# Kernel optimization log

Hardware: AMD Instinct MI355X
Metric: run time of the kernel (lower is better)

The kernel has to match this reference:

```python
import jax, jax.numpy as jnp
import numpy as np

N_PER_GRAPH = 468
B = 32
N = B * N_PER_GRAPH            # 14976 nodes
E = 89600                      # synthetic Delaunay-like directed edges
IN_DIM, HID, OUT, HEADS = 2, 256, 512, 4
NEG_SLOPE = 0.2
EPS = 1e-16


def setup_inputs() -> dict:
    key = jax.random.key(0)
    ks = jax.random.split(key, 12)
    x = jax.random.uniform(ks[0], (N, IN_DIM), dtype=jnp.float32)
    edge_index = jax.random.randint(ks[1], (2, E), 0, N, dtype=jnp.int64)
    batch = jnp.repeat(jnp.arange(B, dtype=jnp.int64), N_PER_GRAPH)
    s1 = 1.0 / np.sqrt(IN_DIM)
    s2 = 1.0 / np.sqrt(HID)
    sg = 1.0 / np.sqrt(OUT)
    return {
        "x": x,
        "edge_index": edge_index,
        "batch": batch,
        # GATConv 1: in_dim -> hidden, heads=4, concat=False
        "W1": jax.random.normal(ks[2], (IN_DIM, HEADS * HID), jnp.float32) * s1,
        "a1_src": jax.random.normal(ks[3], (HEADS, HID), jnp.float32) * s2,
        "a1_dst": jax.random.normal(ks[4], (HEADS, HID), jnp.float32) * s2,
        "b1": jnp.zeros((HID,), jnp.float32),
        # GATConv 2: hidden -> out, heads=4, concat=False
        "W2": jax.random.normal(ks[5], (HID, HEADS * OUT), jnp.float32) * s2,
        "a2_src": jax.random.normal(ks[6], (HEADS, OUT), jnp.float32) * sg,
        "a2_dst": jax.random.normal(ks[7], (HEADS, OUT), jnp.float32) * sg,
        "b2": jnp.zeros((OUT,), jnp.float32),
        # GlobalAttention gate_nn: Linear(out_dim, 1)
        "Wg": jax.random.normal(ks[8], (OUT, 1), jnp.float32) * sg,
        "bg": jnp.zeros((1,), jnp.float32),
    }


def _gat_layer(x, src, dst, W, a_src, a_dst, b, heads, out_ch):
    n = x.shape[0]
    xh = (x @ W).reshape(n, heads, out_ch)            # [N,H,C]
    alpha_s = jnp.einsum("nhc,hc->nh", xh, a_src)     # [N,H]
    alpha_d = jnp.einsum("nhc,hc->nh", xh, a_dst)
    e = alpha_s[src] + alpha_d[dst]                   # [E,H]
    e = jnp.where(e > 0, e, NEG_SLOPE * e)            # leaky_relu(0.2)
    # segment softmax over incoming edges of each destination node
    m = jax.ops.segment_max(e, dst, num_segments=n)
    ex = jnp.exp(e - m[dst])
    denom = jax.ops.segment_sum(ex, dst, num_segments=n)
    alpha = ex / (denom[dst] + EPS)                   # [E,H]
    msg = xh[src] * alpha[:, :, None]                 # [E,H,C]
    out = jax.ops.segment_sum(msg, dst, num_segments=n)  # [N,H,C]
    return out.mean(axis=1) + b                       # concat=False -> head mean


def reference(x, edge_index, batch, W1, a1_src, a1_dst, b1,
              W2, a2_src, a2_dst, b2, Wg, bg):
    n = x.shape[0]
    # PyG GATConv default add_self_loops=True (both layers use the same graph)
    loops = jnp.arange(n, dtype=edge_index.dtype)
    src = jnp.concatenate([edge_index[0], loops])
    dst = jnp.concatenate([edge_index[1], loops])

    h = _gat_layer(x, src, dst, W1, a1_src, a1_dst, b1, HEADS, HID)
    h = jax.nn.relu(h)
    h = _gat_layer(h, src, dst, W2, a2_src, a2_dst, b2, HEADS, OUT)
    h = jax.nn.relu(h)

    # GlobalAttention pooling: gate = Linear(out,1), softmax per graph, weighted sum
    gate = h @ Wg + bg                                # [N,1]
    gm = jax.ops.segment_max(gate, batch, num_segments=B)
    ge = jnp.exp(gate - gm[batch])
    gs = jax.ops.segment_sum(ge, batch, num_segments=B)
    attn = ge / (gs[batch] + EPS)                     # [N,1]
    pooled = jax.ops.segment_sum(attn * h, batch, num_segments=B)  # [B,512]
    return pooled.reshape(-1, 1, OUT)                 # [B,1,512]
```

## Files before the change

### kernel.cpp

```cpp
#include <hip/hip_runtime.h>
#include <hip/hip_bf16.h>
#include <math.h>

#define HEADS 4
#define C1 256
#define C2 512
#define NEG 0.2f
#define EPSF 1e-16f
#define DCAP 64

using bf16x8 = __attribute__((ext_vector_type(8))) short;
using f32x4  = __attribute__((ext_vector_type(4))) float;

__device__ __forceinline__ float lrelu(float e) { return e > 0.f ? e : NEG * e; }

__device__ __forceinline__ unsigned short f2bf(float v) {
    __hip_bfloat16 b = __float2bfloat16(v);
    return *reinterpret_cast<unsigned short*>(&b);
}
__device__ __forceinline__ float bf2f(unsigned short u) {
    __hip_bfloat16 b = *reinterpret_cast<__hip_bfloat16*>(&u);
    return __bfloat162float(b);
}


__global__ __launch_bounds__(256) void k1_prep(
    const float* __restrict__ x, const float* __restrict__ W1,
    const float* __restrict__ a1s, const float* __restrict__ a1d,
    const float* __restrict__ W2, const float* __restrict__ a2s, const float* __restrict__ a2d,
    const int* __restrict__ ei, int E, int N,
    float* __restrict__ as1, float* __restrict__ ad1,
    float* __restrict__ w2a,
    unsigned short* __restrict__ W2t_hi, unsigned short* __restrict__ W2t_lo,
    int* __restrict__ deg, int* __restrict__ bucket)
{
    int b = blockIdx.x, tid = threadIdx.x;
    int wv = tid >> 6, lane = tid & 63;
    if (b < 59) {
        __shared__ float s_w1a[16];
#pragma unroll
        for (int q = 0; q < 4; q++) {
            int o = wv * 4 + q, sd = o >> 3, idx = o & 7, h = idx >> 1, d = idx & 1;
            const float* av = sd ? a1d : a1s;
            float p = 0.f;
            for (int c = lane; c < 256; c += 64) p += W1[d * 1024 + h * 256 + c] * av[h * 256 + c];
#pragma unroll
            for (int m = 32; m >= 1; m >>= 1) p += __shfl_xor(p, m, 64);
            if (lane == 0) s_w1a[o] = p;
        }
        __syncthreads();
        int n = b * 256 + tid;
        if (n < N) {
            float x0 = x[2 * n], x1 = x[2 * n + 1];
            float4 av, dv;
            float* ap = &av.x; float* dp = &dv.x;
#pragma unroll
            for (int h = 0; h < 4; h++) {
                ap[h] = x0 * s_w1a[h * 2] + x1 * s_w1a[h * 2 + 1];
                dp[h] = x0 * s_w1a[8 + h * 2] + x1 * s_w1a[8 + h * 2 + 1];
            }
            *reinterpret_cast<float4*>(&as1[n * 4]) = av;
            *reinterpret_cast<float4*>(&ad1[n * 4]) = dv;
        }
    } else if (b < 67) {
        int bb = b - 59, sd = bb >> 2, h = bb & 3;
        const float* av = sd ? a2d : a2s;
        float gv[8];
#pragma unroll
        for (int q = 0; q < 8; q++) gv[q] = av[h * 512 + lane * 8 + q];
        for (int k = wv; k < 256; k += 4) {
            const float4 w0 = *reinterpret_cast<const float4*>(&W2[(size_t)k * 2048 + h * 512 + lane * 8]);
            const float4 w1 = *reinterpret_cast<const float4*>(&W2[(size_t)k * 2048 + h * 512 + lane * 8 + 4]);
            float p = w0.x*gv[0] + w0.y*gv[1] + w0.z*gv[2] + w0.w*gv[3]
                    + w1.x*gv[4] + w1.y*gv[5] + w1.z*gv[6] + w1.w*gv[7];
#pragma unroll
            for (int m = 32; m >= 1; m >>= 1) p += __shfl_xor(p, m, 64);
            if (lane == 0) w2a[sd * 1024 + h * 256 + k] = p;
        }
    } else if (b < 195) {
        __shared__ float T[64][65];
        int lin = b - 67;
        int kk0 = (lin & 15) * 64, n0 = (lin >> 4) * 64;
        int h = kk0 >> 8, k0 = kk0 & 255;
#pragma unroll
        for (int rr = 0; rr < 16; rr++) {
            int ki = rr * 4 + (tid >> 6), ni = tid & 63;
            T[ki][ni] = W2[(size_t)(k0 + ki) * 2048 + h * 512 + n0 + ni];
        }
        __syncthreads();
#pragma unroll
        for (int rr = 0; rr < 16; rr++) {
            int ni = rr * 4 + (tid >> 6), ki = tid & 63;
            float v = T[ki][ni];
            unsigned short hi = f2bf(v);
            unsigned short lo = f2bf(v - bf2f(hi));
            int rowp = n0 + ni, kg = kk0 + ki;
            int kt = kg >> 5, cb = rowp >> 4;
            int ll = (rowp & 15) | (((kg >> 3) & 3) << 4);
            size_t o = ((size_t)(kt * 32 + cb) * 64 + ll) * 8 + (kg & 7);
            W2t_hi[o] = hi; W2t_lo[o] = lo;
        }
    } else {
        int i = (b - 195) * 256 + tid;
        if (i < E) {
            int s = ei[i], d = ei[E + i];
            int slot = atomicAdd(&deg[d], 1);
            if (slot < DCAP) bucket[d * DCAP + slot] = s;
        }
    }
}

__global__ __launch_bounds__(256) void k4_agg1_h1(
    const float* __restrict__ x, const float* __restrict__ as1, const float* __restrict__ ad1,
    const int* __restrict__ deg, const int* __restrict__ bucket,
    const float* __restrict__ W1, const float* __restrict__ b1, const float* __restrict__ w2a,
    float* __restrict__ h1, float* __restrict__ as2, float* __restrict__ ad2)
{
    int wv = threadIdx.x >> 6, lane = threadIdx.x & 63;
    int n = blockIdx.x * 4 + wv;
    const float4 sa4 = *reinterpret_cast<const float4*>(&as1[n * 4]);
    const float4 da4 = *reinterpret_cast<const float4*>(&ad1[n * 4]);
    const float sa[4] = {sa4.x, sa4.y, sa4.z, sa4.w};
    const float da[4] = {da4.x, da4.y, da4.z, da4.w};
    float acc[8] = {0,0,0,0,0,0,0,0};
    float den[4] = {0,0,0,0};
    int dg = min(deg[n], DCAP);
    for (int i = lane; i < dg; i += 64) {
        int s = bucket[n * DCAP + i];
        const float4 a4 = *reinterpret_cast<const float4*>(&as1[s * 4]);
        const float af[4] = {a4.x, a4.y, a4.z, a4.w};
        const float2 xv = reinterpret_cast<const float2*>(x)[s];
#pragma unroll
        for (int q = 0; q < 4; q++) {
            float w = expf(lrelu(af[q] + da[q]));
            den[q] += w;
            acc[2 * q]     = fmaf(w, xv.x, acc[2 * q]);
            acc[2 * q + 1] = fmaf(w, xv.y, acc[2 * q + 1]);
        }
    }
#pragma unroll
    for (int msk = 1; msk <= 32; msk <<= 1) {
#pragma unroll
        for (int q = 0; q < 8; q++) acc[q] += __shfl_xor(acc[q], msk, 64);
#pragma unroll
        for (int q = 0; q < 4; q++) den[q] += __shfl_xor(den[q], msk, 64);
    }
    const float2 xn = reinterpret_cast<const float2*>(x)[n];
    float xa[8];
#pragma unroll
    for (int q = 0; q < 4; q++) {
        float ws = expf(lrelu(sa[q] + da[q]));
        float dq = den[q] + ws;
        float inv = 1.f / (dq + EPSF);
        xa[2 * q]     = (acc[2 * q]     + ws * xn.x) * inv;
        xa[2 * q + 1] = (acc[2 * q + 1] + ws * xn.y) * inv;
    }
    float t[4] = {0.f, 0.f, 0.f, 0.f};
#pragma unroll
    for (int h = 0; h < 4; h++)
#pragma unroll
        for (int d = 0; d < 2; d++) {
            const float4 w4 = *reinterpret_cast<const float4*>(&W1[d * 1024 + h * 256 + lane * 4]);
            float xx = xa[h * 2 + d];
            t[0] = fmaf(xx, w4.x, t[0]);
            t[1] = fmaf(xx, w4.y, t[1]);
            t[2] = fmaf(xx, w4.z, t[2]);
            t[3] = fmaf(xx, w4.w, t[3]);
        }
    const float4 b4 = *reinterpret_cast<const float4*>(&b1[lane * 4]);
    float v[4];
    v[0] = fmaxf(fmaf(0.25f, t[0], b4.x), 0.f);
    v[1] = fmaxf(fmaf(0.25f, t[1], b4.y), 0.f);
    v[2] = fmaxf(fmaf(0.25f, t[2], b4.z), 0.f);
    v[3] = fmaxf(fmaf(0.25f, t[3], b4.w), 0.f);
    *reinterpret_cast<float4*>(&h1[(size_t)n * 256 + lane * 4]) = make_float4(v[0], v[1], v[2], v[3]);
    float p[8];
#pragma unroll
    for (int o = 0; o < 8; o++) {
        int sd = o >> 2, h = o & 3;
        const float4 w4 = *reinterpret_cast<const float4*>(&w2a[sd * 1024 + h * 256 + lane * 4]);
        p[o] = v[0] * w4.x + v[1] * w4.y + v[2] * w4.z + v[3] * w4.w;
    }
#pragma unroll
    for (int msk = 1; msk <= 32; msk <<= 1)
#pragma unroll
        for (int o = 0; o < 8; o++) p[o] += __shfl_xor(p[o], msk, 64);
    if (lane == 0) {
        *reinterpret_cast<float4*>(&as2[n * 4]) = make_float4(p[0], p[1], p[2], p[3]);
        *reinterpret_cast<float4*>(&ad2[n * 4]) = make_float4(p[4], p[5], p[6], p[7]);
    }
}

__global__ __launch_bounds__(256) void k6_agg2(
    const float* __restrict__ h1, const float* __restrict__ as2, const float* __restrict__ ad2,
    const int* __restrict__ deg, const int* __restrict__ bucket,
    unsigned short* __restrict__ hagg_hi, unsigned short* __restrict__ hagg_lo, int nrb)
{
    int wv = threadIdx.x >> 6, lane = threadIdx.x & 63;
    int n = blockIdx.x * 4 + wv;
    const float4 sa4 = *reinterpret_cast<const float4*>(&as2[n * 4]);
    const float4 da4 = *reinterpret_cast<const float4*>(&ad2[n * 4]);
    const float sa[4] = {sa4.x, sa4.y, sa4.z, sa4.w};
    const float da[4] = {da4.x, da4.y, da4.z, da4.w};
    float den[4], acc[4][4];
    const float4 hs = *reinterpret_cast<const float4*>(&h1[(size_t)n * 256 + lane * 4]);
    const float hv0[4] = {hs.x, hs.y, hs.z, hs.w};
#pragma unroll
    for (int h = 0; h < 4; h++) {
        float ws = expf(lrelu(sa[h] + da[h]));
        den[h] = ws;
#pragma unroll
        for (int q = 0; q < 4; q++) acc[h][q] = ws * hv0[q];
    }
    int dg = min(deg[n], DCAP);
    for (int i = 0; i < dg; i++) {
        int s = bucket[n * DCAP + i];
        const float4 a4 = *reinterpret_cast<const float4*>(&as2[s * 4]);
        const float af[4] = {a4.x, a4.y, a4.z, a4.w};
        const float4 hv = *reinterpret_cast<const float4*>(&h1[(size_t)s * 256 + lane * 4]);
#pragma unroll
        for (int h = 0; h < 4; h++) {
            float w = expf(lrelu(af[h] + da[h]));
            den[h] += w;
            acc[h][0] = fmaf(w, hv.x, acc[h][0]);
            acc[h][1] = fmaf(w, hv.y, acc[h][1]);
            acc[h][2] = fmaf(w, hv.z, acc[h][2]);
            acc[h][3] = fmaf(w, hv.w, acc[h][3]);
        }
    }
    int rb = n >> 4;
    int ll = (n & 15) | (((lane >> 1) & 3) << 4);
    int jj0 = (lane & 1) * 4;
#pragma unroll
    for (int h = 0; h < 4; h++) {
        float inv = 1.f / (den[h] + EPSF);
        ushort4 hi4, lo4;
        unsigned short* hp = &hi4.x; unsigned short* lp = &lo4.x;
#pragma unroll
        for (int q = 0; q < 4; q++) {
            float val = acc[h][q] * inv;
            unsigned short hi = f2bf(val);
            hp[q] = hi;
            lp[q] = f2bf(val - bf2f(hi));
        }
        int kt = h * 8 + (lane >> 3);
        size_t o = ((size_t)(kt * nrb + rb) * 64 + ll) * 8 + jj0;
        *reinterpret_cast<ushort4*>(&hagg_hi[o]) = hi4;
        *reinterpret_cast<ushort4*>(&hagg_lo[o]) = lo4;
    }
}

#define K7_PREF(S, KT) do { int _ao = aoff + (KT) * astep, _bo = boff + (KT) * 2048; \
    _Pragma("unroll") for (int i = 0; i < 4; i++) { \
        S##ah[i] = pAh[_ao + i * 64]; S##al[i] = pAl[_ao + i * 64]; \
        S##bh[i] = pBh[_bo + i * 64]; S##bl[i] = pBl[_bo + i * 64]; } } while (0)

#define K7_MFMA(S) do { _Pragma("unroll") for (int i = 0; i < 4; i++) \
    _Pragma("unroll") for (int jj = 0; jj < 4; jj++) { \
        acc[i][jj] = __builtin_amdgcn_mfma_f32_16x16x32_bf16(S##ah[i], S##bh[jj], acc[i][jj], 0, 0, 0); \
        acc[i][jj] = __builtin_amdgcn_mfma_f32_16x16x32_bf16(S##ah[i], S##bl[jj], acc[i][jj], 0, 0, 0); \
        acc[i][jj] = __builtin_amdgcn_mfma_f32_16x16x32_bf16(S##al[i], S##bh[jj], acc[i][jj], 0, 0, 0); } } while (0)

__global__ __launch_bounds__(256) void k7_gemm2(
    const unsigned short* __restrict__ Ahi, const unsigned short* __restrict__ Alo,
    const unsigned short* __restrict__ Bhi, const unsigned short* __restrict__ Blo,
    const float* __restrict__ b2, const float* __restrict__ Wg,
    float* __restrict__ h2, float* __restrict__ gate, int nrb)
{
    __shared__ float s_gate[128];
    int tid = threadIdx.x, l = tid & 63, wv = tid >> 6;
    int wr = wv >> 1, wc = wv & 1;
    int bid = blockIdx.x, rtile, ctile;
    if (bid < 448) { rtile = (bid & 7) + 8 * (bid >> 5); ctile = (bid >> 3) & 3; }
    else           { int t = bid - 448; rtile = 112 + (t >> 2); ctile = t & 3; }
    int row0 = rtile * 128, col0 = ctile * 128;
    int lm = l & 15, lg = l >> 4;
    if (tid < 128) s_gate[tid] = 0.f;

    const bf16x8* pAh = (const bf16x8*)Ahi;
    const bf16x8* pAl = (const bf16x8*)Alo;
    const bf16x8* pBh = (const bf16x8*)Bhi;
    const bf16x8* pBl = (const bf16x8*)Blo;
    int aoff = (rtile * 8 + wr * 4) * 64 + l;
    int boff = (ctile * 8 + wc * 4) * 64 + l;
    const int astep = nrb * 64;

    f32x4 acc[4][4];
#pragma unroll
    for (int i = 0; i < 4; i++)
#pragma unroll
        for (int jj = 0; jj < 4; jj++) { acc[i][jj][0]=0.f; acc[i][jj][1]=0.f; acc[i][jj][2]=0.f; acc[i][jj][3]=0.f; }

    bf16x8 pah[4], pal[4], pbh[4], pbl[4];
    bf16x8 qah[4], qal[4], qbh[4], qbl[4];
    K7_PREF(p, 0);
    for (int kt = 0; kt < 32; kt += 2) {
        K7_PREF(q, kt + 1);
        K7_MFMA(p);
        if (kt + 2 < 32) K7_PREF(p, kt + 2);
        K7_MFMA(q);
    }
    __syncthreads();

    float b2c[4], wgj[4];
#pragma unroll
    for (int jj = 0; jj < 4; jj++) {
        int col = col0 + wc * 64 + jj * 16 + lm;
        b2c[jj] = b2[col]; wgj[jj] = Wg[col];
    }
#pragma unroll
    for (int i = 0; i < 4; i++) {
#pragma unroll
        for (int r = 0; r < 4; r++) {
            int row = row0 + wr * 64 + i * 16 + lg * 4 + r;
            float g = 0.f;
#pragma unroll
            for (int jj = 0; jj < 4; jj++) {
                float v = fmaxf(fmaf(0.25f, acc[i][jj][r], b2c[jj]), 0.f);
                h2[(size_t)row * 512 + col0 + wc * 64 + jj * 16 + lm] = v;
                g = fmaf(v, wgj[jj], g);
            }
            g += __shfl_xor(g, 1, 64);
            g += __shfl_xor(g, 2, 64);
            g += __shfl_xor(g, 4, 64);
            g += __shfl_xor(g, 8, 64);
            if (lm == 0) atomicAdd(&s_gate[wr * 64 + i * 16 + lg * 4 + r], g);
        }
    }
    __syncthreads();
    if (tid < 128) atomicAdd(&gate[row0 + tid], s_gate[tid]);
}

__global__ __launch_bounds__(256) void k8_pool(
    const float* __restrict__ gate, const float* __restrict__ h2,
    float* __restrict__ out, int npg)
{
    int bq = blockIdx.x, cs = blockIdx.y, tid = threadIdx.x;
    int n0 = bq * npg;
    __shared__ float sw[512];
    __shared__ float sred[4];
    __shared__ float4 sacc[256];
    float part = 0.f;
    for (int i = tid; i < 512; i += 256) {
        float e = (i < npg) ? expf(gate[n0 + i]) : 0.f;
        sw[i] = e; part += e;
    }
#pragma unroll
    for (int m = 32; m >= 1; m >>= 1) part += __shfl_xor(part, m, 64);
    if ((tid & 63) == 0) sred[tid >> 6] = part;
    __syncthreads();
    float inv = 1.f / (sred[0] + sred[1] + sred[2] + sred[3] + EPSF);
    int slot = tid & 31, sub = tid >> 5;
    const float* base = h2 + (size_t)n0 * 512 + cs * 128 + slot * 4;
    float4 acc = make_float4(0.f, 0.f, 0.f, 0.f);
    for (int i = sub; i < npg; i += 8) {
        float w = sw[i];
        const float4 v = *reinterpret_cast<const float4*>(base + (size_t)i * 512);
        acc.x = fmaf(w, v.x, acc.x);
        acc.y = fmaf(w, v.y, acc.y);
        acc.z = fmaf(w, v.z, acc.z);
        acc.w = fmaf(w, v.w, acc.w);
    }
    sacc[tid] = acc;
    __syncthreads();
    if (sub == 0) {
        float4 t = acc;
#pragma unroll
        for (int s2 = 1; s2 < 8; s2++) {
            const float4 o = sacc[s2 * 32 + slot];
            t.x += o.x; t.y += o.y; t.z += o.z; t.w += o.w;
        }
        t.x *= inv; t.y *= inv; t.z *= inv; t.w *= inv;
        *reinterpret_cast<float4*>(&out[(size_t)bq * 512 + cs * 128 + slot * 4]) = t;
    }
}

extern "C" void kernel_launch(void* const* d_in, const int* in_sizes, int n_in,
                              void* d_out, int out_size, void* d_ws, size_t ws_size,
                              hipStream_t stream)
{
    const float* x    = (const float*)d_in[0];
    const int*   ei   = (const int*)d_in[1];
    const float* W1   = (const float*)d_in[3];
    const float* a1s  = (const float*)d_in[4];
    const float* a1d  = (const float*)d_in[5];
    const float* b1   = (const float*)d_in[6];
    const float* W2   = (const float*)d_in[7];
    const float* a2s  = (const float*)d_in[8];
    const float* a2d  = (const float*)d_in[9];
    const float* b2   = (const float*)d_in[10];
    const float* Wg   = (const float*)d_in[11];
    float* out = (float*)d_out;

    const int N = in_sizes[0] / 2;
    const int E = in_sizes[1] / 2;
    const int Bq = out_size / C2;
    const int npg = N / Bq;
    const int nrb = N >> 4;

    char* w = (char*)d_ws;
    size_t off = 0;
    auto alloc = [&](size_t bytes) { void* p = w + off; off += (bytes + 255) & ~(size_t)255; return p; };

    float* h1       = (float*)alloc((size_t)N * 256 * 4);
    float* h2       = (float*)alloc((size_t)N * 512 * 4);
    unsigned short* hagg_hi = (unsigned short*)alloc((size_t)N * 1024 * 2);
    unsigned short* hagg_lo = (unsigned short*)alloc((size_t)N * 1024 * 2);
    unsigned short* W2t_hi  = (unsigned short*)alloc((size_t)512 * 1024 * 2);
    unsigned short* W2t_lo  = (unsigned short*)alloc((size_t)512 * 1024 * 2);
    float* as1   = (float*)alloc((size_t)N * 4 * 4);
    float* ad1   = (float*)alloc((size_t)N * 4 * 4);
    float* as2   = (float*)alloc((size_t)N * 4 * 4);
    float* ad2   = (float*)alloc((size_t)N * 4 * 4);
    int*   deg   = (int*)alloc((size_t)N * 4);
    float* gate  = (float*)alloc((size_t)N * 4);
    float* w2a   = (float*)alloc(2048 * 4);
    int*   bucket = (int*)alloc((size_t)N * DCAP * 4);
    (void)ws_size; (void)n_in;

    const int EB = (E + 255) / 256;

    hipMemsetAsync(deg, 0, (size_t)N * 4 * 2, stream);

    k1_prep<<<195 + EB, 256, 0, stream>>>(x, W1, a1s, a1d, W2, a2s, a2d, ei, E, N,
                                          as1, ad1, w2a, W2t_hi, W2t_lo, deg, bucket);
    k4_agg1_h1<<<N / 4, 256, 0, stream>>>(x, as1, ad1, deg, bucket,
                                          W1, b1, w2a, h1, as2, ad2);
    k6_agg2<<<N / 4, 256, 0, stream>>>(h1, as2, ad2, deg, bucket, hagg_hi, hagg_lo, nrb);
    k7_gemm2<<<468, 256, 0, stream>>>(hagg_hi, hagg_lo, W2t_hi, W2t_lo,
                                      b2, Wg, h2, gate, nrb);
    k8_pool<<<dim3(Bq, 4), 256, 0, stream>>>(gate, h2, out, npg);
}
```

Measured before the change: 264.0 us.

## Stage agg2 output through swizzled LDS for coalesced 16-byte stores

After: 243.8 us. 1.08x faster.

```diff
diff --git a/kernel.cpp b/kernel.cpp
--- a/kernel.cpp
+++ b/kernel.cpp
@@ -191,13 +191,18 @@
     }
 }
 
-__global__ __launch_bounds__(256) void k6_agg2(
+__global__ __launch_bounds__(1024) void k6_agg2(
     const float* __restrict__ h1, const float* __restrict__ as2, const float* __restrict__ ad2,
     const int* __restrict__ deg, const int* __restrict__ bucket,
     unsigned short* __restrict__ hagg_hi, unsigned short* __restrict__ hagg_lo, int nrb)
 {
-    int wv = threadIdx.x >> 6, lane = threadIdx.x & 63;
-    int n = blockIdx.x * 4 + wv;
+    __shared__ unsigned short tH[16 * 1024];
+    __shared__ unsigned short tL[16 * 1024];
+    int tid = threadIdx.x;
+    int wv = tid >> 6, lane = tid & 63;
+    int blk = blockIdx.x;
+    int n = blk * 16 + wv;
+
     const float4 sa4 = *reinterpret_cast<const float4*>(&as2[n * 4]);
     const float4 da4 = *reinterpret_cast<const float4*>(&ad2[n * 4]);
     const float sa[4] = {sa4.x, sa4.y, sa4.z, sa4.w};
@@ -228,9 +233,7 @@
             acc[h][3] = fmaf(w, hv.w, acc[h][3]);
         }
     }
-    int rb = n >> 4;
-    int ll = (n & 15) | (((lane >> 1) & 3) << 4);
-    int jj0 = (lane & 1) * 4;
+    int swz = (wv & 7) << 4;
 #pragma unroll
     for (int h = 0; h < 4; h++) {
         float inv = 1.f / (den[h] + EPSF);
@@ -243,10 +246,22 @@
             hp[q] = hi;
             lp[q] = f2bf(val - bf2f(hi));
         }
-        int kt = h * 8 + (lane >> 3);
-        size_t o = ((size_t)(kt * nrb + rb) * 64 + ll) * 8 + jj0;
-        *reinterpret_cast<ushort4*>(&hagg_hi[o]) = hi4;
-        *reinterpret_cast<ushort4*>(&hagg_lo[o]) = lo4;
+        int bo = (wv * 2048) + ((h * 512 + lane * 8) ^ swz);
+        *reinterpret_cast<ushort4*>((char*)tH + bo) = hi4;
+        *reinterpret_cast<ushort4*>((char*)tL + bo) = lo4;
+    }
+    __syncthreads();
+    int rr = lane & 15, ks = lane >> 4;
+    int rswz = (rr & 7) << 4;
+#pragma unroll
+    for (int t = 0; t < 2; t++) {
+        int kt = wv + t * 16;
+        int lb = (rr * 2048) + ((kt * 64 + ks * 16) ^ rswz);
+        uint4 vh = *reinterpret_cast<const uint4*>((const char*)tH + lb);
+        uint4 vl = *reinterpret_cast<const uint4*>((const char*)tL + lb);
+        size_t go = ((size_t)(kt * nrb + blk) * 64 + lane) * 8;
+        *reinterpret_cast<uint4*>(&hagg_hi[go]) = vh;
+        *reinterpret_cast<uint4*>(&hagg_lo[go]) = vl;
     }
 }
 
@@ -426,7 +441,7 @@
                                           as1, ad1, w2a, W2t_hi, W2t_lo, deg, bucket);
     k4_agg1_h1<<<N / 4, 256, 0, stream>>>(x, as1, ad1, deg, bucket,
                                           W1, b1, w2a, h1, as2, ad2);
-    k6_agg2<<<N / 4, 256, 0, stream>>>(h1, as2, ad2, deg, bucket, hagg_hi, hagg_lo, nrb);
+    k6_agg2<<<N / 16, 1024, 0, stream>>>(h1, as2, ad2, deg, bucket, hagg_hi, hagg_lo, nrb);
     k7_gemm2<<<468, 256, 0, stream>>>(hagg_hi, hagg_lo, W2t_hi, W2t_lo,
                                       b2, Wg, h2, gate, nrb);
     k8_pool<<<dim3(Bq, 4), 256, 0, stream>>>(gate, h2, out, npg);
```
